# Kernel tuning notes

Measured on AMD Instinct MI355X. Metric: run time of the kernel, lower is better.

The kernel has to match this reference:

```python
import jax, jax.numpy as jnp
import numpy as np
from jax.ops import segment_sum, segment_max

N = 20000   # nodes
E = 320000  # edges (no self loops; conv adds them)
G = 64      # graphs in batch
D = 128     # embed dim
H = 64      # GATConv out channels (heads=1)
L = 6       # number of conv/mlp blocks


def setup_inputs() -> dict:
    key = jax.random.key(0)
    ks = jax.random.split(key, 24)
    x_idx = jax.random.randint(ks[0], (N,), 0, 128)
    src = jax.random.randint(ks[1], (E,), 0, N)
    dst = jax.random.randint(ks[2], (E,), 0, N)
    dst = jnp.where(src == dst, (dst + 1) % N, dst)  # remove_self_loops semantics
    edge_index = jnp.stack([src, dst])
    edge_attr_idx = jax.random.randint(ks[3], (E,), 0, 128)
    batch = (jnp.arange(N) * G) // N  # sorted graph ids, ~312 nodes/graph
    s = 0.1
    r = lambda k, shp: jax.random.normal(k, shp, dtype=jnp.float32) * s
    return {
        'x_idx': x_idx, 'edge_index': edge_index, 'edge_attr_idx': edge_attr_idx, 'batch': batch,
        'emb': r(ks[4], (128, D)),
        'conv_W': r(ks[5], (L, D, H)), 'conv_We': r(ks[6], (L, D, H)),
        'conv_att_src': r(ks[7], (L, H)), 'conv_att_dst': r(ks[8], (L, H)),
        'conv_att_edge': r(ks[9], (L, H)), 'conv_b': jnp.zeros((L, H), jnp.float32),
        'mlp_W1': r(ks[10], (L, H, H)), 'mlp_b1': jnp.zeros((L, H), jnp.float32),
        'mlp_W2': r(ks[11], (L, H, H)), 'mlp_b2': jnp.zeros((L, H), jnp.float32),
        'mlp_W3': r(ks[12], (L, H, D)), 'mlp_b3': jnp.zeros((L, D), jnp.float32),
        'g1_W1': r(ks[13], (D, H)), 'g1_b1': jnp.zeros((H,), jnp.float32),
        'g1_W2': r(ks[14], (H, 1)), 'g1_b2': jnp.zeros((1,), jnp.float32),
        'g2_W1': r(ks[15], (D, H)), 'g2_b1': jnp.zeros((H,), jnp.float32),
        'g2_W2': r(ks[16], (H, D)), 'g2_b2': jnp.zeros((D,), jnp.float32),
        'p_W1': r(ks[17], (D, H)), 'p_b1': jnp.zeros((H,), jnp.float32),
        'p_W2': r(ks[18], (H, H)), 'p_b2': jnp.zeros((H,), jnp.float32),
        'p_W3': r(ks[19], (H, 1)), 'p_b3': jnp.zeros((1,), jnp.float32),
    }


def _mlp3(x, W1, b1, W2, b2, W3, b3):
    h = jax.nn.relu(x @ W1 + b1)
    h = jax.nn.relu(h @ W2 + b2)
    return h @ W3 + b3


def reference(x_idx, edge_index, edge_attr_idx, batch, emb, conv_W, conv_We,
              conv_att_src, conv_att_dst, conv_att_edge, conv_b,
              mlp_W1, mlp_b1, mlp_W2, mlp_b2, mlp_W3, mlp_b3,
              g1_W1, g1_b1, g1_W2, g1_b2, g2_W1, g2_b1, g2_W2, g2_b2,
              p_W1, p_b1, p_W2, p_b2, p_W3, p_b3):
    n = x_idx.shape[0]
    x = emb[x_idx]                 # [N,128]
    e = emb[edge_attr_idx]         # [E,128]
    src, dst = edge_index[0], edge_index[1]
    # add_self_loops with fill_value='mean': loop attr = mean of incoming edge attrs
    deg = segment_sum(jnp.ones((e.shape[0],), x.dtype), dst, num_segments=n)
    loop_attr = segment_sum(e, dst, num_segments=n) / jnp.maximum(deg, 1.0)[:, None]
    e_full = jnp.concatenate([e, loop_attr], axis=0)             # [E+N,128]
    ar = jnp.arange(n)
    src_f = jnp.concatenate([src, ar])
    dst_f = jnp.concatenate([dst, ar])

    def gat_conv(x, i):
        h = x @ conv_W[i]                       # [N,64]
        ep = e_full @ conv_We[i]                # [E+N,64]
        a_s = h @ conv_att_src[i]               # [N]
        a_d = h @ conv_att_dst[i]               # [N]
        a_e = ep @ conv_att_edge[i]             # [E+N]
        logit = jax.nn.leaky_relu(a_s[src_f] + a_d[dst_f] + a_e, 0.2)
        m = segment_max(logit, dst_f, num_segments=n)
        w = jnp.exp(logit - m[dst_f])
        denom = segment_sum(w, dst_f, num_segments=n)
        alpha = w / denom[dst_f]
        out = segment_sum(h[src_f] * alpha[:, None], dst_f, num_segments=n)
        return out + conv_b[i]

    jkn = []
    for i in range(L):  # dropout is identity at inference
        x = gat_conv(x, i)
        x = _mlp3(x, mlp_W1[i], mlp_b1[i], mlp_W2[i], mlp_b2[i], mlp_W3[i], mlp_b3[i])
        jkn.append(x)
    jkn = jnp.stack(jkn)                                  # [6,N,128]
    ms = jnp.sqrt(jnp.sum(jnp.square(jkn), axis=2))       # [6,N]
    ni = jnp.argmax(ms, axis=0)                           # [N]
    feature = jnp.take_along_axis(jkn, ni[None, :, None], axis=0)[0]  # [N,128]

    # per-graph attention pooling (vectorized over the per-graph loop)
    h1 = (jax.nn.relu(feature @ g1_W1 + g1_b1) @ g1_W2 + g1_b2)[:, 0]  # [N]
    m = segment_max(h1, batch, num_segments=G)
    w = jnp.exp(h1 - m[batch])
    attn = w / segment_sum(w, batch, num_segments=G)[batch]            # softmax per graph
    h2 = jax.nn.relu(feature @ g2_W1 + g2_b1) @ g2_W2 + g2_b2          # [N,128]
    counts = segment_sum(jnp.ones((n,), feature.dtype), batch, num_segments=G)
    hg = segment_sum(attn[:, None] * h2, batch, num_segments=G) / counts[:, None]  # [G,128]

    out = _mlp3(hg, p_W1, p_b1, p_W2, p_b2, p_W3, p_b3)   # [G,1]
    return out[:, 0]
```

## Files before the change

### kernel.cpp

```cpp
#include <hip/hip_runtime.h>
#include <math.h>

__device__ __forceinline__ float lrelu(float x){ return x > 0.0f ? x : 0.2f*x; }
__device__ __forceinline__ float bcastf(float v, int l){
    return __int_as_float(__builtin_amdgcn_readlane(__float_as_int(v), l));
}


__global__ void k_count(const int* __restrict__ dst, int* __restrict__ cnt, int E){
    int e = blockIdx.x*256 + threadIdx.x;
    if(e < E) atomicAdd(&cnt[dst[e]], 1);
}

__global__ __launch_bounds__(1024) void k_scan(const int* __restrict__ cnt, int* __restrict__ rowptr, int n){
    __shared__ int ws[16];
    __shared__ int carrysh;
    int t = threadIdx.x, lane = t & 63, wv = t >> 6;
    if(t==0){ carrysh = 0; rowptr[0] = 0; }
    __syncthreads();
    for(int base=0; base<n; base+=1024){
        int i = base + t;
        int v = (i<n) ? cnt[i] : 0;
        int s = v;
        #pragma unroll
        for(int off=1; off<64; off<<=1){ int u = __shfl_up(s, off, 64); if(lane>=off) s += u; }
        if(lane==63) ws[wv] = s;
        __syncthreads();
        if(t < 16){
            int u = ws[t];
            #pragma unroll
            for(int off=1; off<16; off<<=1){ int u2 = __shfl_up(u, off, 16); if(t>=off) u += u2; }
            ws[t] = u;
        }
        __syncthreads();
        int carry = carrysh;
        int wbase = wv ? ws[wv-1] : 0;
        if(i<n) rowptr[i+1] = carry + wbase + s;
        int total = ws[15];
        __syncthreads();
        if(t==0) carrysh = carry + total;
        __syncthreads();
    }
}

__global__ void k_scatter(const int* __restrict__ dst, const int* __restrict__ rowptr,
                          int* __restrict__ cnt2, int* __restrict__ eid, int E){
    int e = blockIdx.x*256 + threadIdx.x;
    if(e >= E) return;
    int d = dst[e];
    int p = rowptr[d] + atomicAdd(&cnt2[d], 1);
    eid[p] = e;
}

__global__ __launch_bounds__(256) void k_sortb(const int* __restrict__ rowptr, int* __restrict__ eid, int n){
    int node = blockIdx.x*4 + (threadIdx.x>>6);
    if(node >= n) return;
    int lane = threadIdx.x & 63;
    int b = rowptr[node], e = rowptr[node+1];
    int nj = e - b;
    if(nj <= 1) return;
    if(nj <= 64){
        int v = (lane < nj) ? eid[b+lane] : 0x7fffffff;
        for(int k=2; k<=64; k<<=1){
            for(int j=k>>1; j>0; j>>=1){
                int vv = __shfl_xor(v, j, 64);
                bool up = ((lane & k) == 0);
                bool lower = ((lane & j) == 0);
                int mn = min(v,vv), mx = max(v,vv);
                v = (lower == up) ? mn : mx;
            }
        }
        if(lane < nj) eid[b+lane] = v;
    } else if(lane == 0){
        for(int i=b+1; i<e; i++){
            int key = eid[i]; int j = i-1;
            while(j>=b && eid[j] > key){ eid[j+1] = eid[j]; j--; }
            eid[j+1] = key;
        }
    }
}

__global__ __launch_bounds__(256) void k_ae(const int* __restrict__ eid, const int* __restrict__ src,
                     const int* __restrict__ eattr, const float* __restrict__ emb,
                     const float* __restrict__ We, const float* __restrict__ atte,
                     int* __restrict__ csrsrc, float* __restrict__ ae, int E){
    __shared__ float wv[6*128];
    for(int i=threadIdx.x; i<768; i+=256){
        int l = i>>7, k = i&127;
        const float* w = We + ((size_t)l*128 + k)*64;
        const float* a = atte + l*64;
        float s = 0.f;
        #pragma unroll 8
        for(int c=0;c<64;c++) s += w[c]*a[c];
        wv[i] = s;
    }
    __syncthreads();
    int p = blockIdx.x*256 + threadIdx.x;
    if(p >= E) return;
    int e = eid[p];
    csrsrc[p] = src[e];
    const float4* er = (const float4*)(emb + (size_t)eattr[e]*128);
    float acc[6] = {0,0,0,0,0,0};
    for(int k=0;k<32;k++){
        float4 v = er[k];
        #pragma unroll
        for(int l=0;l<6;l++){
            const float* w = wv + l*128 + k*4;
            acc[l] += v.x*w[0] + v.y*w[1] + v.z*w[2] + v.w*w[3];
        }
    }
    #pragma unroll
    for(int l=0;l<6;l++) ae[(size_t)l*E + p] = acc[l];
}


__global__ __launch_bounds__(512) void k_hx(const int* __restrict__ xidx, const float* __restrict__ emb,
        const float* __restrict__ W, const float* __restrict__ atts, const float* __restrict__ attd,
        float* __restrict__ h, float* __restrict__ as_, float* __restrict__ ad_, int n){
    __shared__ float xs[64][129];
    __shared__ float hs[64][65];
    __shared__ float redA[8][64], redB[8][64];
    int base = blockIdx.x*64;
    int t = threadIdx.x;
    {
        int r = t>>3, c0 = (t&7)*16;
        if(base + r < n){
            const float4* srcp = (const float4*)(emb + (size_t)xidx[base+r]*128 + c0);
            #pragma unroll
            for(int q=0;q<4;q++){
                float4 v = srcp[q];
                xs[r][c0+q*4+0]=v.x; xs[r][c0+q*4+1]=v.y; xs[r][c0+q*4+2]=v.z; xs[r][c0+q*4+3]=v.w;
            }
        } else {
            #pragma unroll
            for(int q=0;q<16;q++) xs[r][c0+q] = 0.f;
        }
    }
    __syncthreads();
    int lane = t & 63;
    int wid = __builtin_amdgcn_readfirstlane(t >> 6);
    int cb = wid*8;
    float acc[8] = {0,0,0,0,0,0,0,0};
    for(int k=0;k<128;k++){
        float xv = xs[lane][k];
        #pragma unroll
        for(int cc=0;cc<8;cc++) acc[cc] = fmaf(xv, W[k*64 + cb + cc], acc[cc]);
    }
    float pa=0.f, pd=0.f;
    #pragma unroll
    for(int cc=0;cc<8;cc++){
        hs[lane][cb+cc] = acc[cc];
        pa += acc[cc]*atts[cb+cc];
        pd += acc[cc]*attd[cb+cc];
    }
    redA[wid][lane]=pa; redB[wid][lane]=pd;
    __syncthreads();
    {
        int r = t>>3, c0 = (t&7)*8;
        if(base + r < n){
            float* dst = h + (size_t)(base+r)*64 + c0;
            #pragma unroll
            for(int q=0;q<8;q++) dst[q] = hs[r][c0+q];
        }
    }
    if(t < 64 && base + t < n){
        float sa=0.f, sd=0.f;
        #pragma unroll
        for(int w=0;w<8;w++){ sa += redA[w][t]; sd += redB[w][t]; }
        as_[base+t] = sa; ad_[base+t] = sd;
    }
}


__global__ __launch_bounds__(256) void k_gat(const float* __restrict__ h,
        const float* __restrict__ as_, const float* __restrict__ ad_,
        const float* __restrict__ ae, const int* __restrict__ rowptr,
        const int* __restrict__ csrsrc, const float* __restrict__ bias,
        float* __restrict__ o, int n){
    int node = blockIdx.x*4 + (threadIdx.x>>6);
    if(node >= n) return;
    int lane = threadIdx.x & 63;
    int b = rowptr[node], e = rowptr[node+1];
    float adv = ad_[node];
    float m = -1e30f, d = 0.f, sumae = 0.f;
    float a0=0.f, a1=0.f, a2=0.f, a3=0.f;
    for(int j0=b; j0<e; j0+=64){
        int nj = min(64, e-j0);
        int sj = 0; float aev = 0.f, lg = -1e30f;
        if(lane < nj){
            sj  = csrsrc[j0+lane];
            aev = ae[j0+lane];
            lg  = lrelu(as_[sj] + adv + aev);
        }
        float cm = lg, sa = aev;
        #pragma unroll
        for(int off=32; off; off>>=1){ cm = fmaxf(cm, __shfl_xor(cm,off,64)); sa += __shfl_xor(sa,off,64); }
        sumae += sa;
        float nm = fmaxf(m, cm);
        float w = (lane<nj) ? expf(lg-nm) : 0.f;
        float ws = w;
        #pragma unroll
        for(int off=32; off; off>>=1) ws += __shfl_xor(ws,off,64);
        float scale = (m > -1e29f) ? expf(m-nm) : 0.f;
        d = d*scale + ws;
        a0*=scale; a1*=scale; a2*=scale; a3*=scale;
        int j = 0;
        for(; j+3<nj; j+=4){
            a0 = fmaf(bcastf(w,j+0), h[(size_t)__builtin_amdgcn_readlane(sj,j+0)*64 + lane], a0);
            a1 = fmaf(bcastf(w,j+1), h[(size_t)__builtin_amdgcn_readlane(sj,j+1)*64 + lane], a1);
            a2 = fmaf(bcastf(w,j+2), h[(size_t)__builtin_amdgcn_readlane(sj,j+2)*64 + lane], a2);
            a3 = fmaf(bcastf(w,j+3), h[(size_t)__builtin_amdgcn_readlane(sj,j+3)*64 + lane], a3);
        }
        for(; j<nj; j++)
            a0 = fmaf(bcastf(w,j), h[(size_t)__builtin_amdgcn_readlane(sj,j)*64 + lane], a0);
        m = nm;
    }
    int deg = e - b;
    float ael = sumae / fmaxf((float)deg, 1.f);
    float ls = lrelu(as_[node] + adv + ael);
    float nm = fmaxf(m, ls);
    float scale = (m > -1e29f) ? expf(m-nm) : 0.f;
    float wl = expf(ls-nm);
    d = d*scale + wl;
    float acc = (a0+a1)+(a2+a3);
    acc = acc*scale + wl*h[(size_t)node*64 + lane];
    o[(size_t)node*64 + lane] = acc/d + bias[lane];
}


__global__ __launch_bounds__(512) void k_dense(
    const float* __restrict__ o,
    const float* __restrict__ W1, const float* __restrict__ b1,
    const float* __restrict__ W2, const float* __restrict__ b2,
    const float* __restrict__ W3, const float* __restrict__ b3,
    float* __restrict__ bestF, float* __restrict__ bestMs, int layer,
    const float* __restrict__ Wn, const float* __restrict__ atts, const float* __restrict__ attd,
    float* __restrict__ hn, float* __restrict__ asn, float* __restrict__ adn_,
    const float* __restrict__ A, const float* __restrict__ g1b1,
    const float* __restrict__ w2, const float* __restrict__ g1b2,
    const float* __restrict__ B, const float* __restrict__ g2b1,
    const float* __restrict__ C, const float* __restrict__ g2b2,
    float* __restrict__ h1, float* __restrict__ h2,
    int n, int last)
{
    __shared__ float o_s[64][65];
    __shared__ float t1[64][65];
    __shared__ float xs[64][129];
    __shared__ float redA[8][64], redB[8][64];
    __shared__ unsigned char updf[64];
    int base = blockIdx.x*64;
    int t = threadIdx.x, lane = t & 63;
    int wid = __builtin_amdgcn_readfirstlane(t >> 6);

    {
        int r = t>>3, c0 = (t&7)*8;
        if(base + r < n){
            const float4* srcp = (const float4*)(o + (size_t)(base+r)*64 + c0);
            float4 v0 = srcp[0], v1 = srcp[1];
            o_s[r][c0+0]=v0.x; o_s[r][c0+1]=v0.y; o_s[r][c0+2]=v0.z; o_s[r][c0+3]=v0.w;
            o_s[r][c0+4]=v1.x; o_s[r][c0+5]=v1.y; o_s[r][c0+6]=v1.z; o_s[r][c0+7]=v1.w;
        } else {
            #pragma unroll
            for(int q=0;q<8;q++) o_s[r][c0+q] = 0.f;
        }
    }
    __syncthreads();

    {
        int cb = wid*8;
        float acc[8];
        #pragma unroll
        for(int cc=0;cc<8;cc++) acc[cc] = b1[cb+cc];
        for(int k=0;k<64;k++){
            float ov = o_s[lane][k];
            #pragma unroll
            for(int cc=0;cc<8;cc++) acc[cc] = fmaf(ov, W1[k*64 + cb + cc], acc[cc]);
        }
        #pragma unroll
        for(int cc=0;cc<8;cc++) t1[lane][cb+cc] = fmaxf(acc[cc], 0.f);
    }
    __syncthreads();

    {
        int cb = wid*8;
        float acc[8];
        #pragma unroll
        for(int cc=0;cc<8;cc++) acc[cc] = b2[cb+cc];
        for(int k=0;k<64;k++){
            float tv = t1[lane][k];
            #pragma unroll
            for(int cc=0;cc<8;cc++) acc[cc] = fmaf(tv, W2[k*64 + cb + cc], acc[cc]);
        }
        __syncthreads();
        #pragma unroll
        for(int cc=0;cc<8;cc++) o_s[lane][cb+cc] = fmaxf(acc[cc], 0.f);
    }
    __syncthreads();

    {
        int cb = wid*16;
        float acc[16];
        #pragma unroll
        for(int cc=0;cc<16;cc++) acc[cc] = b3[cb+cc];
        for(int k=0;k<64;k++){
            float tv = o_s[lane][k];
            #pragma unroll
            for(int cc=0;cc<16;cc++) acc[cc] = fmaf(tv, W3[k*128 + cb + cc], acc[cc]);
        }
        float ms = 0.f;
        #pragma unroll
        for(int cc=0;cc<16;cc++){ xs[lane][cb+cc] = acc[cc]; ms += acc[cc]*acc[cc]; }
        redA[wid][lane] = ms;
    }
    __syncthreads();

    if(t < 64){
        int node = base + t; bool u = false;
        if(node < n){
            float ms = 0.f;
            #pragma unroll
            for(int w=0;w<8;w++) ms += redA[w][t];
            u = (layer==0) || (ms > bestMs[node]);
            if(u) bestMs[node] = ms;
        }
        updf[t] = u ? 1 : 0;
    }
    __syncthreads();

    if(!last){
        {
            int r = t>>3, c0 = (t&7)*16;
            if(updf[r] && base + r < n){
                float* dst = bestF + (size_t)(base+r)*128 + c0;
                #pragma unroll
                for(int q=0;q<16;q++) dst[q] = xs[r][c0+q];
            }
        }
        {
            int cb = wid*8;
            float acc[8] = {0,0,0,0,0,0,0,0};
            for(int k=0;k<128;k++){
                float xv = xs[lane][k];
                #pragma unroll
                for(int cc=0;cc<8;cc++) acc[cc] = fmaf(xv, Wn[k*64 + cb + cc], acc[cc]);
            }
            float pa=0.f, pd=0.f;
            #pragma unroll
            for(int cc=0;cc<8;cc++){
                t1[lane][cb+cc] = acc[cc];
                pa += acc[cc]*atts[cb+cc];
                pd += acc[cc]*attd[cb+cc];
            }
            redA[wid][lane]=pa; redB[wid][lane]=pd;
        }
        __syncthreads();
        {
            int r = t>>3, c0 = (t&7)*8;
            if(base + r < n){
                float* dst = hn + (size_t)(base+r)*64 + c0;
                #pragma unroll
                for(int q=0;q<8;q++) dst[q] = t1[r][c0+q];
            }
        }
        if(t < 64 && base + t < n){
            float sa=0.f, sd=0.f;
            #pragma unroll
            for(int w=0;w<8;w++){ sa += redA[w][t]; sd += redB[w][t]; }
            asn[base+t] = sa; adn_[base+t] = sd;
        }
        return;
    }

    {
        int r = t>>3, c0 = (t&7)*16;
        if(!updf[r] && base + r < n){
            const float4* srcp = (const float4*)(bestF + (size_t)(base+r)*128 + c0);
            #pragma unroll
            for(int q=0;q<4;q++){
                float4 v = srcp[q];
                xs[r][c0+q*4+0]=v.x; xs[r][c0+q*4+1]=v.y; xs[r][c0+q*4+2]=v.z; xs[r][c0+q*4+3]=v.w;
            }
        }
    }
    __syncthreads();
    if(wid < 4){
        int cb = wid*16;
        float acc[16];
        #pragma unroll
        for(int cc=0;cc<16;cc++) acc[cc] = g1b1[cb+cc];
        for(int k=0;k<128;k++){
            float fv = xs[lane][k];
            #pragma unroll
            for(int cc=0;cc<16;cc++) acc[cc] = fmaf(fv, A[k*64 + cb + cc], acc[cc]);
        }
        float pp = 0.f;
        #pragma unroll
        for(int cc=0;cc<16;cc++) pp += fmaxf(acc[cc],0.f)*w2[cb+cc];
        redA[wid][lane] = pp;
    } else {
        int cb = (wid-4)*16;
        float acc[16];
        #pragma unroll
        for(int cc=0;cc<16;cc++) acc[cc] = g2b1[cb+cc];
        for(int k=0;k<128;k++){
            float fv = xs[lane][k];
            #pragma unroll
            for(int cc=0;cc<16;cc++) acc[cc] = fmaf(fv, B[k*64 + cb + cc], acc[cc]);
        }
        #pragma unroll
        for(int cc=0;cc<16;cc++) t1[lane][cb+cc] = fmaxf(acc[cc],0.f);
    }
    __syncthreads();
    if(t < 64 && base + t < n)
        h1[base+t] = redA[0][t]+redA[1][t]+redA[2][t]+redA[3][t] + g1b2[0];
    {
        int cb = wid*16;
        float acc[16];
        #pragma unroll
        for(int cc=0;cc<16;cc++) acc[cc] = g2b2[cb+cc];
        for(int k=0;k<64;k++){
            float tv = t1[lane][k];
            #pragma unroll
            for(int cc=0;cc<16;cc++) acc[cc] = fmaf(tv, C[k*128 + cb + cc], acc[cc]);
        }
        __syncthreads();
        #pragma unroll
        for(int cc=0;cc<16;cc++) xs[lane][cb+cc] = acc[cc];
    }
    __syncthreads();
    {
        int r = t>>3, c0 = (t&7)*16;
        if(base + r < n){
            float* dst = h2 + (size_t)(base+r)*128 + c0;
            #pragma unroll
            for(int q=0;q<16;q++) dst[q] = xs[r][c0+q];
        }
    }
}


__global__ __launch_bounds__(128) void k_pool2(const float* __restrict__ h1, const float* __restrict__ h2,
                      float* __restrict__ wbuf,
                      const float* __restrict__ pW1, const float* __restrict__ pb1,
                      const float* __restrict__ pW2, const float* __restrict__ pb2,
                      const float* __restrict__ pW3, const float* __restrict__ pb3,
                      float* __restrict__ out, int n, int G){
    __shared__ float sh[128];
    __shared__ float hgrow[128];
    int g = blockIdx.x, tid = threadIdx.x;
    int start = (g*n + G-1)/G, end = ((g+1)*n + G-1)/G;
    float lm = -1e30f;
    for(int i=start+tid; i<end; i+=128) lm = fmaxf(lm, h1[i]);
    sh[tid]=lm; __syncthreads();
    for(int off=64; off; off>>=1){ if(tid<off) sh[tid]=fmaxf(sh[tid],sh[tid+off]); __syncthreads(); }
    float m = sh[0]; __syncthreads();
    float lsum = 0.f;
    for(int i=start+tid; i<end; i+=128){ float w = expf(h1[i]-m); wbuf[i]=w; lsum+=w; }
    sh[tid]=lsum; __syncthreads();
    for(int off=64; off; off>>=1){ if(tid<off) sh[tid]+=sh[tid+off]; __syncthreads(); }
    float denom = sh[0];
    float a0=0.f,a1=0.f,a2=0.f,a3=0.f;
    int i = start;
    for(; i+3<end; i+=4){
        a0 = fmaf(wbuf[i+0], h2[(size_t)(i+0)*128 + tid], a0);
        a1 = fmaf(wbuf[i+1], h2[(size_t)(i+1)*128 + tid], a1);
        a2 = fmaf(wbuf[i+2], h2[(size_t)(i+2)*128 + tid], a2);
        a3 = fmaf(wbuf[i+3], h2[(size_t)(i+3)*128 + tid], a3);
    }
    for(; i<end; i++) a0 = fmaf(wbuf[i], h2[(size_t)i*128 + tid], a0);
    float acc = (a0+a1)+(a2+a3);
    hgrow[tid] = acc/denom/(float)(end-start);
    __syncthreads();
    if(tid < 64){
        float t1v = pb1[tid];
        for(int k=0;k<128;k++) t1v = fmaf(hgrow[k], pW1[k*64+tid], t1v);
        t1v = fmaxf(t1v, 0.f);
        float t2v = pb2[tid];
        for(int k=0;k<64;k++) t2v = fmaf(__shfl(t1v,k,64), pW2[k*64+tid], t2v);
        t2v = fmaxf(t2v, 0.f);
        float s = t2v * pW3[tid];
        #pragma unroll
        for(int off=32; off; off>>=1) s += __shfl_xor(s,off,64);
        if(tid==0) out[g] = s + pb3[0];
    }
}

extern "C" void kernel_launch(void* const* d_in, const int* in_sizes, int n_in,
                              void* d_out, int out_size, void* d_ws, size_t ws_size,
                              hipStream_t stream){
    const int*   x_idx   = (const int*)  d_in[0];
    const int*   eindex  = (const int*)  d_in[1];
    const int*   eattr   = (const int*)  d_in[2];
    const float* emb     = (const float*)d_in[4];
    const float* conv_W  = (const float*)d_in[5];
    const float* conv_We = (const float*)d_in[6];
    const float* att_src = (const float*)d_in[7];
    const float* att_dst = (const float*)d_in[8];
    const float* att_edg = (const float*)d_in[9];
    const float* conv_b  = (const float*)d_in[10];
    const float* mW1 = (const float*)d_in[11]; const float* mb1 = (const float*)d_in[12];
    const float* mW2 = (const float*)d_in[13]; const float* mb2 = (const float*)d_in[14];
    const float* mW3 = (const float*)d_in[15]; const float* mb3 = (const float*)d_in[16];
    const float* g1W1= (const float*)d_in[17]; const float* g1b1= (const float*)d_in[18];
    const float* g1W2= (const float*)d_in[19]; const float* g1b2= (const float*)d_in[20];
    const float* g2W1= (const float*)d_in[21]; const float* g2b1= (const float*)d_in[22];
    const float* g2W2= (const float*)d_in[23]; const float* g2b2= (const float*)d_in[24];
    const float* pW1 = (const float*)d_in[25]; const float* pb1 = (const float*)d_in[26];
    const float* pW2 = (const float*)d_in[27]; const float* pb2 = (const float*)d_in[28];
    const float* pW3 = (const float*)d_in[29]; const float* pb3 = (const float*)d_in[30];

    const int N = in_sizes[0];
    const int E = in_sizes[2];
    const int G = out_size;
    const int* src = eindex;
    const int* dst = eindex + E;
    const int NT = (N + 63) / 64;
    const int NW = (N + 3) / 4;

    char* p = (char*)d_ws;
    auto alloc = [&](size_t bytes)->void*{ void* r = (void*)p; p += (bytes + 255) & ~(size_t)255; return r; };
    float* h      = (float*)alloc((size_t)N*64*4);
    float* o      = (float*)alloc((size_t)N*64*4);
    float* bestF  = (float*)alloc((size_t)N*128*4);
    float* h2buf  = (float*)alloc((size_t)N*128*4);
    float* bestMs = (float*)alloc((size_t)N*4);
    float* as_    = (float*)alloc((size_t)N*4);
    float* ad_    = (float*)alloc((size_t)N*4);
    float* ae     = (float*)alloc((size_t)6*E*4);
    float* h1     = (float*)alloc((size_t)N*4);
    int*   cnt    = (int*)  alloc((size_t)N*4);
    int*   cnt2   = (int*)  alloc((size_t)N*4);
    int*   rowptr = (int*)  alloc((size_t)(N+1)*4);
    int*   eid    = (int*)  alloc((size_t)E*4);
    int*   csrsrc = (int*)  alloc((size_t)E*4);

    hipMemsetAsync(cnt,  0, (size_t)N*4, stream);
    hipMemsetAsync(cnt2, 0, (size_t)N*4, stream);

    k_count<<<(E+255)/256, 256, 0, stream>>>(dst, cnt, E);
    k_scan<<<1, 1024, 0, stream>>>(cnt, rowptr, N);
    k_scatter<<<(E+255)/256, 256, 0, stream>>>(dst, rowptr, cnt2, eid, E);
    k_sortb<<<NW, 256, 0, stream>>>(rowptr, eid, N);
    k_ae<<<(E+255)/256, 256, 0, stream>>>(eid, src, eattr, emb, conv_We, att_edg, csrsrc, ae, E);
    k_hx<<<NT, 512, 0, stream>>>(x_idx, emb, conv_W, att_src, att_dst, h, as_, ad_, N);

    for(int l=0; l<6; l++){
        int last = (l==5) ? 1 : 0;
        const float* Wn   = last ? conv_W  : conv_W  + (size_t)(l+1)*8192;
        const float* atsn = last ? att_src : att_src + (l+1)*64;
        const float* atdn = last ? att_dst : att_dst + (l+1)*64;
        k_gat<<<NW, 256, 0, stream>>>(h, as_, ad_, ae + (size_t)l*E, rowptr, csrsrc, conv_b + l*64, o, N);
        k_dense<<<NT, 512, 0, stream>>>(o,
            mW1 + (size_t)l*4096, mb1 + l*64, mW2 + (size_t)l*4096, mb2 + l*64,
            mW3 + (size_t)l*8192, mb3 + l*128,
            bestF, bestMs, l,
            Wn, atsn, atdn,
            h, as_, ad_,
            g1W1, g1b1, g1W2, g1b2, g2W1, g2b1, g2W2, g2b2,
            h1, h2buf,
            N, last);
    }

    k_pool2<<<G, 128, 0, stream>>>(h1, h2buf, bestMs,
            pW1, pb1, pW2, pb2, pW3, pb3, (float*)d_out, N, G);
}
```

Before: 480.9 us.

## Precompute per-attribute edge attention table and rewrite dense kernels wave-per-8-nodes

Replaces the per-edge attention logit array with a 6x128 table indexed by edge attribute id, and packs the source index and attribute id into one int per edge. This removes the 6*E float buffer and its reads in the GAT kernel. The dense MLP and projection kernels are rewritten so each wavefront handles 8 nodes in registers, broadcasting activations with readlane instead of staging through shared memory and barriers. The packing assumes node ids fit in 17 bits, and the new code keeps more values in registers per thread.

```diff
diff --git a/kernel.cpp b/kernel.cpp
--- a/kernel.cpp
+++ b/kernel.cpp
@@ -4,6 +4,11 @@
 __device__ __forceinline__ float lrelu(float x){ return x > 0.0f ? x : 0.2f*x; }
 __device__ __forceinline__ float bcastf(float v, int l){
     return __int_as_float(__builtin_amdgcn_readlane(__float_as_int(v), l));
+}
+__device__ __forceinline__ float wsum(float v){
+    #pragma unroll
+    for(int off=32; off; off>>=1) v += __shfl_xor(v, off, 64);
+    return v;
 }
 
 
@@ -80,103 +85,91 @@
     }
 }
 
-__global__ __launch_bounds__(256) void k_ae(const int* __restrict__ eid, const int* __restrict__ src,
-                     const int* __restrict__ eattr, const float* __restrict__ emb,
-                     const float* __restrict__ We, const float* __restrict__ atte,
-                     int* __restrict__ csrsrc, float* __restrict__ ae, int E){
-    __shared__ float wv[6*128];
-    for(int i=threadIdx.x; i<768; i+=256){
-        int l = i>>7, k = i&127;
+__global__ void k_pack(const int* __restrict__ eid, const int* __restrict__ src,
+                       const int* __restrict__ eattr, int* __restrict__ packed, int E){
+    int p = blockIdx.x*256 + threadIdx.x;
+    if(p >= E) return;
+    int e = eid[p];
+    packed[p] = src[e] | (eattr[e] << 17);
+}
+
+__global__ __launch_bounds__(768) void k_table(const float* __restrict__ We, const float* __restrict__ atte,
+                                               const float* __restrict__ emb, float* __restrict__ T){
+    __shared__ float wv[768];
+    int t = threadIdx.x;
+    {
+        int l = t>>7, k = t&127;
         const float* w = We + ((size_t)l*128 + k)*64;
         const float* a = atte + l*64;
         float s = 0.f;
         #pragma unroll 8
         for(int c=0;c<64;c++) s += w[c]*a[c];
-        wv[i] = s;
+        wv[t] = s;
     }
     __syncthreads();
-    int p = blockIdx.x*256 + threadIdx.x;
-    if(p >= E) return;
-    int e = eid[p];
-    csrsrc[p] = src[e];
-    const float4* er = (const float4*)(emb + (size_t)eattr[e]*128);
-    float acc[6] = {0,0,0,0,0,0};
+    int l = t>>7, a = t&127;
+    const float4* er = (const float4*)(emb + (size_t)a*128);
+    const float* w = wv + l*128;
+    float acc = 0.f;
     for(int k=0;k<32;k++){
         float4 v = er[k];
-        #pragma unroll
-        for(int l=0;l<6;l++){
-            const float* w = wv + l*128 + k*4;
-            acc[l] += v.x*w[0] + v.y*w[1] + v.z*w[2] + v.w*w[3];
-        }
-    }
-    #pragma unroll
-    for(int l=0;l<6;l++) ae[(size_t)l*E + p] = acc[l];
-}
-
-
-__global__ __launch_bounds__(512) void k_hx(const int* __restrict__ xidx, const float* __restrict__ emb,
+        acc += v.x*w[k*4+0] + v.y*w[k*4+1] + v.z*w[k*4+2] + v.w*w[k*4+3];
+    }
+    T[l*128 + a] = acc;
+}
+
+
+__global__ __launch_bounds__(256) void k_hx(const int* __restrict__ xidx, const float* __restrict__ emb,
         const float* __restrict__ W, const float* __restrict__ atts, const float* __restrict__ attd,
         float* __restrict__ h, float* __restrict__ as_, float* __restrict__ ad_, int n){
-    __shared__ float xs[64][129];
-    __shared__ float hs[64][65];
-    __shared__ float redA[8][64], redB[8][64];
-    int base = blockIdx.x*64;
-    int t = threadIdx.x;
-    {
-        int r = t>>3, c0 = (t&7)*16;
-        if(base + r < n){
-            const float4* srcp = (const float4*)(emb + (size_t)xidx[base+r]*128 + c0);
-            #pragma unroll
-            for(int q=0;q<4;q++){
-                float4 v = srcp[q];
-                xs[r][c0+q*4+0]=v.x; xs[r][c0+q*4+1]=v.y; xs[r][c0+q*4+2]=v.z; xs[r][c0+q*4+3]=v.w;
-            }
-        } else {
-            #pragma unroll
-            for(int q=0;q<16;q++) xs[r][c0+q] = 0.f;
-        }
-    }
-    __syncthreads();
-    int lane = t & 63;
-    int wid = __builtin_amdgcn_readfirstlane(t >> 6);
-    int cb = wid*8;
-    float acc[8] = {0,0,0,0,0,0,0,0};
-    for(int k=0;k<128;k++){
-        float xv = xs[lane][k];
-        #pragma unroll
-        for(int cc=0;cc<8;cc++) acc[cc] = fmaf(xv, W[k*64 + cb + cc], acc[cc]);
-    }
-    float pa=0.f, pd=0.f;
+    int t = threadIdx.x, lane = t & 63;
+    int base = blockIdx.x*32 + (t>>6)*8;
+    if(base >= n) return;
+    int nv = min(8, n - base);
+
+    float xv0[8], xv1[8];
     #pragma unroll
-    for(int cc=0;cc<8;cc++){
-        hs[lane][cb+cc] = acc[cc];
-        pa += acc[cc]*atts[cb+cc];
-        pd += acc[cc]*attd[cb+cc];
-    }
-    redA[wid][lane]=pa; redB[wid][lane]=pd;
-    __syncthreads();
-    {
-        int r = t>>3, c0 = (t&7)*8;
-        if(base + r < n){
-            float* dst = h + (size_t)(base+r)*64 + c0;
-            #pragma unroll
-            for(int q=0;q<8;q++) dst[q] = hs[r][c0+q];
-        }
-    }
-    if(t < 64 && base + t < n){
-        float sa=0.f, sd=0.f;
-        #pragma unroll
-        for(int w=0;w<8;w++){ sa += redA[w][t]; sd += redB[w][t]; }
-        as_[base+t] = sa; ad_[base+t] = sd;
+    for(int nn=0;nn<8;nn++){
+        if(nn < nv){
+            int xi = xidx[base+nn];
+            xv0[nn] = emb[(size_t)xi*128 + lane];
+            xv1[nn] = emb[(size_t)xi*128 + 64 + lane];
+        } else { xv0[nn]=0.f; xv1[nn]=0.f; }
+    }
+    float hv[8] = {0,0,0,0,0,0,0,0};
+    #pragma unroll 2
+    for(int k=0;k<64;k++){
+        float w = W[k*64 + lane];
+        #pragma unroll
+        for(int nn=0;nn<8;nn++) hv[nn] = fmaf(bcastf(xv0[nn],k), w, hv[nn]);
+    }
+    #pragma unroll 2
+    for(int k=0;k<64;k++){
+        float w = W[(k+64)*64 + lane];
+        #pragma unroll
+        for(int nn=0;nn<8;nn++) hv[nn] = fmaf(bcastf(xv1[nn],k), w, hv[nn]);
+    }
+    float atl = atts[lane], adl = attd[lane];
+    #pragma unroll
+    for(int nn=0;nn<8;nn++){
+        float sa = wsum(hv[nn]*atl);
+        float sd = wsum(hv[nn]*adl);
+        if(nn < nv){
+            h[(size_t)(base+nn)*64 + lane] = hv[nn];
+            if(lane==0){ as_[base+nn] = sa; ad_[base+nn] = sd; }
+        }
     }
 }
 
 
 __global__ __launch_bounds__(256) void k_gat(const float* __restrict__ h,
         const float* __restrict__ as_, const float* __restrict__ ad_,
-        const float* __restrict__ ae, const int* __restrict__ rowptr,
-        const int* __restrict__ csrsrc, const float* __restrict__ bias,
+        const float* __restrict__ T, const int* __restrict__ packed,
+        const int* __restrict__ rowptr, const float* __restrict__ bias,
         float* __restrict__ o, int n){
+    __shared__ float Tl[128];
+    if(threadIdx.x < 128) Tl[threadIdx.x] = T[threadIdx.x];
+    __syncthreads();
     int node = blockIdx.x*4 + (threadIdx.x>>6);
     if(node >= n) return;
     int lane = threadIdx.x & 63;
@@ -188,8 +181,9 @@
         int nj = min(64, e-j0);
         int sj = 0; float aev = 0.f, lg = -1e30f;
         if(lane < nj){
-            sj  = csrsrc[j0+lane];
-            aev = ae[j0+lane];
+            int pk = packed[j0+lane];
+            sj  = pk & 0x1FFFF;
+            aev = Tl[pk >> 17];
             lg  = lrelu(as_[sj] + adv + aev);
         }
         float cm = lg, sa = aev;
@@ -228,7 +222,7 @@
 }
 
 
-__global__ __launch_bounds__(512) void k_dense(
+__global__ __launch_bounds__(256) void k_dense(
     const float* __restrict__ o,
     const float* __restrict__ W1, const float* __restrict__ b1,
     const float* __restrict__ W2, const float* __restrict__ b2,
@@ -243,197 +237,183 @@
     float* __restrict__ h1, float* __restrict__ h2,
     int n, int last)
 {
-    __shared__ float o_s[64][65];
-    __shared__ float t1[64][65];
-    __shared__ float xs[64][129];
-    __shared__ float redA[8][64], redB[8][64];
-    __shared__ unsigned char updf[64];
-    int base = blockIdx.x*64;
     int t = threadIdx.x, lane = t & 63;
-    int wid = __builtin_amdgcn_readfirstlane(t >> 6);
-
-    {
-        int r = t>>3, c0 = (t&7)*8;
-        if(base + r < n){
-            const float4* srcp = (const float4*)(o + (size_t)(base+r)*64 + c0);
-            float4 v0 = srcp[0], v1 = srcp[1];
-            o_s[r][c0+0]=v0.x; o_s[r][c0+1]=v0.y; o_s[r][c0+2]=v0.z; o_s[r][c0+3]=v0.w;
-            o_s[r][c0+4]=v1.x; o_s[r][c0+5]=v1.y; o_s[r][c0+6]=v1.z; o_s[r][c0+7]=v1.w;
-        } else {
-            #pragma unroll
-            for(int q=0;q<8;q++) o_s[r][c0+q] = 0.f;
-        }
-    }
-    __syncthreads();
-
-    {
-        int cb = wid*8;
-        float acc[8];
-        #pragma unroll
-        for(int cc=0;cc<8;cc++) acc[cc] = b1[cb+cc];
-        for(int k=0;k<64;k++){
-            float ov = o_s[lane][k];
-            #pragma unroll
-            for(int cc=0;cc<8;cc++) acc[cc] = fmaf(ov, W1[k*64 + cb + cc], acc[cc]);
-        }
-        #pragma unroll
-        for(int cc=0;cc<8;cc++) t1[lane][cb+cc] = fmaxf(acc[cc], 0.f);
-    }
-    __syncthreads();
-
-    {
-        int cb = wid*8;
-        float acc[8];
-        #pragma unroll
-        for(int cc=0;cc<8;cc++) acc[cc] = b2[cb+cc];
-        for(int k=0;k<64;k++){
-            float tv = t1[lane][k];
-            #pragma unroll
-            for(int cc=0;cc<8;cc++) acc[cc] = fmaf(tv, W2[k*64 + cb + cc], acc[cc]);
-        }
-        __syncthreads();
-        #pragma unroll
-        for(int cc=0;cc<8;cc++) o_s[lane][cb+cc] = fmaxf(acc[cc], 0.f);
-    }
-    __syncthreads();
-
-    {
-        int cb = wid*16;
-        float acc[16];
-        #pragma unroll
-        for(int cc=0;cc<16;cc++) acc[cc] = b3[cb+cc];
-        for(int k=0;k<64;k++){
-            float tv = o_s[lane][k];
-            #pragma unroll
-            for(int cc=0;cc<16;cc++) acc[cc] = fmaf(tv, W3[k*128 + cb + cc], acc[cc]);
-        }
-        float ms = 0.f;
-        #pragma unroll
-        for(int cc=0;cc<16;cc++){ xs[lane][cb+cc] = acc[cc]; ms += acc[cc]*acc[cc]; }
-        redA[wid][lane] = ms;
-    }
-    __syncthreads();
-
-    if(t < 64){
-        int node = base + t; bool u = false;
-        if(node < n){
-            float ms = 0.f;
-            #pragma unroll
-            for(int w=0;w<8;w++) ms += redA[w][t];
-            u = (layer==0) || (ms > bestMs[node]);
-            if(u) bestMs[node] = ms;
-        }
-        updf[t] = u ? 1 : 0;
-    }
-    __syncthreads();
+    int base = blockIdx.x*32 + (t>>6)*8;
+    if(base >= n) return;
+    int nv = min(8, n - base);
+
+    float ov[8];
+    #pragma unroll
+    for(int nn=0;nn<8;nn++) ov[nn] = (nn<nv) ? o[(size_t)(base+nn)*64 + lane] : 0.f;
+
+    float t1[8];
+    {
+        float bb = b1[lane];
+        #pragma unroll
+        for(int nn=0;nn<8;nn++) t1[nn] = bb;
+        #pragma unroll 4
+        for(int k=0;k<64;k++){
+            float w = W1[k*64 + lane];
+            #pragma unroll
+            for(int nn=0;nn<8;nn++) t1[nn] = fmaf(bcastf(ov[nn],k), w, t1[nn]);
+        }
+        #pragma unroll
+        for(int nn=0;nn<8;nn++) t1[nn] = fmaxf(t1[nn], 0.f);
+    }
+
+    float t2[8];
+    {
+        float bb = b2[lane];
+        #pragma unroll
+        for(int nn=0;nn<8;nn++) t2[nn] = bb;
+        #pragma unroll 4
+        for(int k=0;k<64;k++){
+            float w = W2[k*64 + lane];
+            #pragma unroll
+            for(int nn=0;nn<8;nn++) t2[nn] = fmaf(bcastf(t1[nn],k), w, t2[nn]);
+        }
+        #pragma unroll
+        for(int nn=0;nn<8;nn++) t2[nn] = fmaxf(t2[nn], 0.f);
+    }
+
+    float xp0[8], xp1[8];
+    {
+        float ba = b3[lane], bb = b3[lane+64];
+        #pragma unroll
+        for(int nn=0;nn<8;nn++){ xp0[nn]=ba; xp1[nn]=bb; }
+        #pragma unroll 2
+        for(int k=0;k<64;k++){
+            float w0 = C ? 0.f : 0.f;
+            (void)w0;
+            float wa = W3[k*128 + lane];
+            float wb = W3[k*128 + 64 + lane];
+            #pragma unroll
+            for(int nn=0;nn<8;nn++){
+                float s = bcastf(t2[nn],k);
+                xp0[nn] = fmaf(s, wa, xp0[nn]);
+                xp1[nn] = fmaf(s, wb, xp1[nn]);
+            }
+        }
+    }
+
+    float msv[8]; bool upd[8];
+    #pragma unroll
+    for(int nn=0;nn<8;nn++){
+        float p = wsum(xp0[nn]*xp0[nn] + xp1[nn]*xp1[nn]);
+        msv[nn] = p;
+        float prev = -1e30f;
+        if(layer > 0 && nn < nv) prev = bestMs[base+nn];
+        upd[nn] = (layer==0) || (p > prev);
+    }
 
     if(!last){
-        {
-            int r = t>>3, c0 = (t&7)*16;
-            if(updf[r] && base + r < n){
-                float* dst = bestF + (size_t)(base+r)*128 + c0;
-                #pragma unroll
-                for(int q=0;q<16;q++) dst[q] = xs[r][c0+q];
+        #pragma unroll
+        for(int nn=0;nn<8;nn++){
+            if(nn<nv && upd[nn]){
+                bestF[(size_t)(base+nn)*128 + lane]      = xp0[nn];
+                bestF[(size_t)(base+nn)*128 + 64 + lane] = xp1[nn];
+                if(lane==0) bestMs[base+nn] = msv[nn];
             }
         }
-        {
-            int cb = wid*8;
-            float acc[8] = {0,0,0,0,0,0,0,0};
-            for(int k=0;k<128;k++){
-                float xv = xs[lane][k];
-                #pragma unroll
-                for(int cc=0;cc<8;cc++) acc[cc] = fmaf(xv, Wn[k*64 + cb + cc], acc[cc]);
+        float hv[8] = {0,0,0,0,0,0,0,0};
+        #pragma unroll 2
+        for(int k=0;k<64;k++){
+            float w = Wn[k*64 + lane];
+            #pragma unroll
+            for(int nn=0;nn<8;nn++) hv[nn] = fmaf(bcastf(xp0[nn],k), w, hv[nn]);
+        }
+        #pragma unroll 2
+        for(int k=0;k<64;k++){
+            float w = Wn[(k+64)*64 + lane];
+            #pragma unroll
+            for(int nn=0;nn<8;nn++) hv[nn] = fmaf(bcastf(xp1[nn],k), w, hv[nn]);
+        }
+        float atl = atts[lane], adl = attd[lane];
+        #pragma unroll
+        for(int nn=0;nn<8;nn++){
+            float sa = wsum(hv[nn]*atl);
+            float sd = wsum(hv[nn]*adl);
+            if(nn<nv){
+                hn[(size_t)(base+nn)*64 + lane] = hv[nn];
+                if(lane==0){ asn[base+nn] = sa; adn_[base+nn] = sd; }
             }
-            float pa=0.f, pd=0.f;
-            #pragma unroll
-            for(int cc=0;cc<8;cc++){
-                t1[lane][cb+cc] = acc[cc];
-                pa += acc[cc]*atts[cb+cc];
-                pd += acc[cc]*attd[cb+cc];
+        }
+        return;
+    }
+
+    #pragma unroll
+    for(int nn=0;nn<8;nn++){
+        if(nn<nv && !upd[nn]){
+            xp0[nn] = bestF[(size_t)(base+nn)*128 + lane];
+            xp1[nn] = bestF[(size_t)(base+nn)*128 + 64 + lane];
+        }
+    }
+    {
+        float p1[8];
+        float bb = g1b1[lane];
+        #pragma unroll
+        for(int nn=0;nn<8;nn++) p1[nn] = bb;
+        #pragma unroll 2
+        for(int k=0;k<64;k++){
+            float w = A[k*64 + lane];
+            #pragma unroll
+            for(int nn=0;nn<8;nn++) p1[nn] = fmaf(bcastf(xp0[nn],k), w, p1[nn]);
+        }
+        #pragma unroll 2
+        for(int k=0;k<64;k++){
+            float w = A[(k+64)*64 + lane];
+            #pragma unroll
+            for(int nn=0;nn<8;nn++) p1[nn] = fmaf(bcastf(xp1[nn],k), w, p1[nn]);
+        }
+        float w2l = w2[lane], bout = g1b2[0];
+        #pragma unroll
+        for(int nn=0;nn<8;nn++){
+            float s = wsum(fmaxf(p1[nn],0.f)*w2l);
+            if(nn<nv && lane==0) h1[base+nn] = s + bout;
+        }
+    }
+    float p2[8];
+    {
+        float bb = g2b1[lane];
+        #pragma unroll
+        for(int nn=0;nn<8;nn++) p2[nn] = bb;
+        #pragma unroll 2
+        for(int k=0;k<64;k++){
+            float w = B[k*64 + lane];
+            #pragma unroll
+            for(int nn=0;nn<8;nn++) p2[nn] = fmaf(bcastf(xp0[nn],k), w, p2[nn]);
+        }
+        #pragma unroll 2
+        for(int k=0;k<64;k++){
+            float w = B[(k+64)*64 + lane];
+            #pragma unroll
+            for(int nn=0;nn<8;nn++) p2[nn] = fmaf(bcastf(xp1[nn],k), w, p2[nn]);
+        }
+        #pragma unroll
+        for(int nn=0;nn<8;nn++) p2[nn] = fmaxf(p2[nn], 0.f);
+    }
+    {
+        float r0[8], r1[8];
+        float ba = g2b2[lane], bb = g2b2[lane+64];
+        #pragma unroll
+        for(int nn=0;nn<8;nn++){ r0[nn]=ba; r1[nn]=bb; }
+        #pragma unroll 2
+        for(int k=0;k<64;k++){
+            float wa = C[k*128 + lane];
+            float wb = C[k*128 + 64 + lane];
+            #pragma unroll
+            for(int nn=0;nn<8;nn++){
+                float s = bcastf(p2[nn],k);
+                r0[nn] = fmaf(s, wa, r0[nn]);
+                r1[nn] = fmaf(s, wb, r1[nn]);
             }
-            redA[wid][lane]=pa; redB[wid][lane]=pd;
-        }
-        __syncthreads();
-        {
-            int r = t>>3, c0 = (t&7)*8;
-            if(base + r < n){
-                float* dst = hn + (size_t)(base+r)*64 + c0;
-                #pragma unroll
-                for(int q=0;q<8;q++) dst[q] = t1[r][c0+q];
+        }
+        #pragma unroll
+        for(int nn=0;nn<8;nn++){
+            if(nn<nv){
+                h2[(size_t)(base+nn)*128 + lane]      = r0[nn];
+                h2[(size_t)(base+nn)*128 + 64 + lane] = r1[nn];
             }
-        }
-        if(t < 64 && base + t < n){
-            float sa=0.f, sd=0.f;
-            #pragma unroll
-            for(int w=0;w<8;w++){ sa += redA[w][t]; sd += redB[w][t]; }
-            asn[base+t] = sa; adn_[base+t] = sd;
-        }
-        return;
-    }
-
-    {
-        int r = t>>3, c0 = (t&7)*16;
-        if(!updf[r] && base + r < n){
-            const float4* srcp = (const float4*)(bestF + (size_t)(base+r)*128 + c0);
-            #pragma unroll
-            for(int q=0;q<4;q++){
-                float4 v = srcp[q];
-                xs[r][c0+q*4+0]=v.x; xs[r][c0+q*4+1]=v.y; xs[r][c0+q*4+2]=v.z; xs[r][c0+q*4+3]=v.w;
-            }
-        }
-    }
-    __syncthreads();
-    if(wid < 4){
-        int cb = wid*16;
-        float acc[16];
-        #pragma unroll
-        for(int cc=0;cc<16;cc++) acc[cc] = g1b1[cb+cc];
-        for(int k=0;k<128;k++){
-            float fv = xs[lane][k];
-            #pragma unroll
-            for(int cc=0;cc<16;cc++) acc[cc] = fmaf(fv, A[k*64 + cb + cc], acc[cc]);
-        }
-        float pp = 0.f;
-        #pragma unroll
-        for(int cc=0;cc<16;cc++) pp += fmaxf(acc[cc],0.f)*w2[cb+cc];
-        redA[wid][lane] = pp;
-    } else {
-        int cb = (wid-4)*16;
-        float acc[16];
-        #pragma unroll
-        for(int cc=0;cc<16;cc++) acc[cc] = g2b1[cb+cc];
-        for(int k=0;k<128;k++){
-            float fv = xs[lane][k];
-            #pragma unroll
-            for(int cc=0;cc<16;cc++) acc[cc] = fmaf(fv, B[k*64 + cb + cc], acc[cc]);
-        }
-        #pragma unroll
-        for(int cc=0;cc<16;cc++) t1[lane][cb+cc] = fmaxf(acc[cc],0.f);
-    }
-    __syncthreads();
-    if(t < 64 && base + t < n)
-        h1[base+t] = redA[0][t]+redA[1][t]+redA[2][t]+redA[3][t] + g1b2[0];
-    {
-        int cb = wid*16;
-        float acc[16];
-        #pragma unroll
-        for(int cc=0;cc<16;cc++) acc[cc] = g2b2[cb+cc];
-        for(int k=0;k<64;k++){
-            float tv = t1[lane][k];
-            #pragma unroll
-            for(int cc=0;cc<16;cc++) acc[cc] = fmaf(tv, C[k*128 + cb + cc], acc[cc]);
-        }
-        __syncthreads();
-        #pragma unroll
-        for(int cc=0;cc<16;cc++) xs[lane][cb+cc] = acc[cc];
-    }
-    __syncthreads();
-    {
-        int r = t>>3, c0 = (t&7)*16;
-        if(base + r < n){
-            float* dst = h2 + (size_t)(base+r)*128 + c0;
-            #pragma unroll
-            for(int q=0;q<16;q++) dst[q] = xs[r][c0+q];
         }
     }
 }
@@ -514,8 +494,8 @@
     const int G = out_size;
     const int* src = eindex;
     const int* dst = eindex + E;
-    const int NT = (N + 63) / 64;
     const int NW = (N + 3) / 4;
+    const int ND = (N + 31) / 32;
 
     char* p = (char*)d_ws;
     auto alloc = [&](size_t bytes)->void*{ void* r = (void*)p; p += (bytes + 255) & ~(size_t)255; return r; };
@@ -526,13 +506,13 @@
     float* bestMs = (float*)alloc((size_t)N*4);
     float* as_    = (float*)alloc((size_t)N*4);
     float* ad_    = (float*)alloc((size_t)N*4);
-    float* ae     = (float*)alloc((size_t)6*E*4);
+    float* Tbuf   = (float*)alloc(6*128*4);
     float* h1     = (float*)alloc((size_t)N*4);
     int*   cnt    = (int*)  alloc((size_t)N*4);
     int*   cnt2   = (int*)  alloc((size_t)N*4);
     int*   rowptr = (int*)  alloc((size_t)(N+1)*4);
     int*   eid    = (int*)  alloc((size_t)E*4);
-    int*   csrsrc = (int*)  alloc((size_t)E*4);
+    int*   packed = (int*)  alloc((size_t)E*4);
 
     hipMemsetAsync(cnt,  0, (size_t)N*4, stream);
     hipMemsetAsync(cnt2, 0, (size_t)N*4, stream);
@@ -541,16 +521,17 @@
     k_scan<<<1, 1024, 0, stream>>>(cnt, rowptr, N);
     k_scatter<<<(E+255)/256, 256, 0, stream>>>(dst, rowptr, cnt2, eid, E);
     k_sortb<<<NW, 256, 0, stream>>>(rowptr, eid, N);
-    k_ae<<<(E+255)/256, 256, 0, stream>>>(eid, src, eattr, emb, conv_We, att_edg, csrsrc, ae, E);
-    k_hx<<<NT, 512, 0, stream>>>(x_idx, emb, conv_W, att_src, att_dst, h, as_, ad_, N);
+    k_pack<<<(E+255)/256, 256, 0, stream>>>(eid, src, eattr, packed, E);
+    k_table<<<1, 768, 0, stream>>>(conv_We, att_edg, emb, Tbuf);
+    k_hx<<<ND, 256, 0, stream>>>(x_idx, emb, conv_W, att_src, att_dst, h, as_, ad_, N);
 
     for(int l=0; l<6; l++){
         int last = (l==5) ? 1 : 0;
         const float* Wn   = last ? conv_W  : conv_W  + (size_t)(l+1)*8192;
         const float* atsn = last ? att_src : att_src + (l+1)*64;
         const float* atdn = last ? att_dst : att_dst + (l+1)*64;
-        k_gat<<<NW, 256, 0, stream>>>(h, as_, ad_, ae + (size_t)l*E, rowptr, csrsrc, conv_b + l*64, o, N);
-        k_dense<<<NT, 512, 0, stream>>>(o,
+        k_gat<<<NW, 256, 0, stream>>>(h, as_, ad_, Tbuf + l*128, packed, rowptr, conv_b + l*64, o, N);
+        k_dense<<<ND, 256, 0, stream>>>(o,
             mW1 + (size_t)l*4096, mb1 + l*64, mW2 + (size_t)l*4096, mb2 + l*64,
             mW3 + (size_t)l*8192, mb3 + l*128,
             bestF, bestMs, l,
```

Result: slower. 603.9 us (+25.6%).
